# Optimization experiments

Hardware: AMD Instinct MI355X
Metric: run time of the kernel (lower is better)

## Reference

```python
import jax, jax.numpy as jnp
import numpy as np

CH = 96          # channels
E = 2 * CH       # expand_ratio * channels = 192
S = 16           # ssm_state_dim
LN_EPS = 1e-3    # keras LayerNormalization default epsilon


def setup_inputs() -> dict:
    key = jax.random.key(0)
    ks = jax.random.split(key, 8)
    inputs = jax.random.normal(ks[0], (8, 128, 128, CH), dtype=jnp.float32)
    scale = 0.05
    return {
        "inputs": inputs,
        "ln_gamma": jnp.ones((CH,), jnp.float32),
        "ln_beta": jnp.zeros((CH,), jnp.float32),
        "W_expand": jax.random.normal(ks[1], (CH, E), jnp.float32) * scale,
        "W_gate": jax.random.normal(ks[2], (CH, E), jnp.float32) * scale,
        "A": jax.random.normal(ks[3], (E, S), jnp.float32) * scale,
        "B": jax.random.normal(ks[4], (E, S), jnp.float32) * scale,
        "C": jax.random.normal(ks[5], (E, S), jnp.float32) * scale,
        "D": jnp.zeros((E,), jnp.float32),
        "W_out": jax.random.normal(ks[6], (E, CH), jnp.float32) * scale,
    }


def _layernorm(x, gamma, beta):
    mean = jnp.mean(x, axis=-1, keepdims=True)
    var = jnp.mean(jnp.square(x - mean), axis=-1, keepdims=True)
    return (x - mean) / jnp.sqrt(var + LN_EPS) * gamma + beta


def _ssm_scan(u, A, B, C, D):
    # u: [Bn, H, W, E]; diagonal linear recurrence along W with per-(channel,state) params.
    Bn, H, W, Ech = u.shape
    u_t = jnp.moveaxis(u, 2, 0)  # [W, Bn, H, E]

    def step(state, u_w):  # state: [Bn, H, E, S], u_w: [Bn, H, E]
        st = state * A + u_w[..., None] * B               # [Bn, H, E, S]
        # Faithful to the TF code: u*D is broadcast over the state dim
        # before the sum, contributing S * u * D.
        y = jnp.sum(st * C, axis=-1) + S * u_w * D        # [Bn, H, E]
        return st, y

    init = jnp.zeros((Bn, H, Ech, S), dtype=u.dtype)
    _, y = jax.lax.scan(step, init, u_t)                  # y: [W, Bn, H, E]
    return jnp.moveaxis(y, 0, 2)                          # [Bn, H, W, E]


def reference(inputs, ln_gamma, ln_beta, W_expand, W_gate, A, B, C, D, W_out):
    x = _layernorm(inputs, ln_gamma, ln_beta)
    x_proj = jnp.einsum("bhwc,ce->bhwe", x, W_expand)
    gate = jax.nn.sigmoid(jnp.einsum("bhwc,ce->bhwe", x, W_gate))
    ssm_out = _ssm_scan(x_proj, A, B, C, D)
    gated = gate * ssm_out
    return jnp.einsum("bhwe,ec->bhwc", gated, W_out)
```

## Files before the change

kernel.cpp:

```cpp
#include <hip/hip_runtime.h>
#include <math.h>

#define CHN 96
#define EC 192
#define SS 16
#define WPIX 128
#define TILE 16
#define HPX 64
#define NTILES (HPX / TILE)
#define KT 8
#define HALO (KT - 1)
#define NT 192

__global__ void prep_scale(const float* __restrict__ We,
                           const float* __restrict__ Wg,
                           const float* __restrict__ gamma,
                           float* __restrict__ WeP,
                           float* __restrict__ WgP) {
    const int c = blockIdx.x;
    const int e = threadIdx.x;
    const float g = gamma[c];
    WeP[c * EC + e] = g * We[c * EC + e];
    WgP[c * EC + e] = g * Wg[c * EC + e];
}

__global__ void prep_sums(const float* __restrict__ We,
                          const float* __restrict__ Wg,
                          const float* __restrict__ beta,
                          const float* __restrict__ WeP,
                          const float* __restrict__ WgP,
                          float* __restrict__ se, float* __restrict__ be,
                          float* __restrict__ sg, float* __restrict__ bg) {
    const int e = threadIdx.x;
    float s1 = 0.f, b1 = 0.f, s2 = 0.f, b2 = 0.f;
    for (int c = 0; c < CHN; ++c) {
        s1 += WeP[c * EC + e];
        s2 += WgP[c * EC + e];
        b1 += beta[c] * We[c * EC + e];
        b2 += beta[c] * Wg[c * EC + e];
    }
    se[e] = s1; be[e] = b1; sg[e] = s2; bg[e] = b2;
}

#define LOADW(W, c4) {                                         \
    W##0 = wep[((c4) * 4 + 0) * EC]; W##1 = wep[((c4) * 4 + 1) * EC]; \
    W##2 = wep[((c4) * 4 + 2) * EC]; W##3 = wep[((c4) * 4 + 3) * EC]; \
    W##4 = wgp[((c4) * 4 + 0) * EC]; W##5 = wgp[((c4) * 4 + 1) * EC]; \
    W##6 = wgp[((c4) * 4 + 2) * EC]; W##7 = wgp[((c4) * 4 + 3) * EC]; }

#define FMAB(W, c4) {                                          \
    _Pragma("unroll")                                          \
    for (int w = 0; w < TILE; ++w) {                           \
        float4 xv = *(const float4*)(xtile + w * CHN + (c4) * 4); \
        accp[w] = fmaf(xv.x, W##0, accp[w]);                   \
        accp[w] = fmaf(xv.y, W##1, accp[w]);                   \
        accp[w] = fmaf(xv.z, W##2, accp[w]);                   \
        accp[w] = fmaf(xv.w, W##3, accp[w]);                   \
        accg[w] = fmaf(xv.x, W##4, accg[w]);                   \
        accg[w] = fmaf(xv.y, W##5, accg[w]);                   \
        accg[w] = fmaf(xv.z, W##6, accg[w]);                   \
        accg[w] = fmaf(xv.w, W##7, accg[w]); } }

#define LOADO(W, ch) {                                         \
    _Pragma("unroll")                                          \
    for (int k = 0; k < 16; ++k) W[k] = Wo[((ch) * 16 + k) * CHN + co]; }

#define FMAO(W, ch) {                                          \
    _Pragma("unroll")                                          \
    for (int j = 0; j < 8; ++j) {                              \
        const float* gp_ = &gs[wgr * 8 + j][(ch) * 16];        \
        _Pragma("unroll")                                      \
        for (int k4 = 0; k4 < 4; ++k4) {                       \
            float4 gv = *(const float4*)(gp_ + k4 * 4);        \
            acco[j] = fmaf(gv.x, W[k4 * 4 + 0], acco[j]);      \
            acco[j] = fmaf(gv.y, W[k4 * 4 + 1], acco[j]);      \
            acco[j] = fmaf(gv.z, W[k4 * 4 + 2], acco[j]);      \
            acco[j] = fmaf(gv.w, W[k4 * 4 + 3], acco[j]); } } }

__global__ __launch_bounds__(NT, 6)
void mamba_fused(const float* __restrict__ in,
                 const float* __restrict__ WeP,
                 const float* __restrict__ WgP,
                 const float* __restrict__ sev,
                 const float* __restrict__ bev,
                 const float* __restrict__ sgv,
                 const float* __restrict__ bgv,
                 const float* __restrict__ Ap,
                 const float* __restrict__ Bp,
                 const float* __restrict__ Cp,
                 const float* __restrict__ Dp,
                 const float* __restrict__ Wo,
                 float* __restrict__ out) {
    __shared__ float gs[TILE][EC];
    __shared__ float2 stats[TILE];
    __shared__ float2 stats_h[HALO];

    const int t = threadIdx.x;
    const int row  = blockIdx.x >> 1;
    const int half = blockIdx.x & 1;
    const float* inrow = in + (size_t)row * WPIX * CHN;

    const int e = t;
    const float* wep = WeP + e;
    const float* wgp = WgP + e;
    const float se_r = sev[e], be_r = bev[e], sg_r = sgv[e], bg_r = bgv[e];

    float h[KT];
    {
        #pragma unroll
        for (int k = 0; k < KT; ++k) h[k] = 0.f;
        for (int s = 0; s < SS; ++s) {
            const float a = Ap[e * SS + s];
            float p = Bp[e * SS + s] * Cp[e * SS + s];
            #pragma unroll
            for (int k = 0; k < KT; ++k) { h[k] += p; p *= a; }
        }
        h[0] += (float)SS * Dp[e];
    }

    const int px  = t >> 3;
    const int ln  = t & 7;
    const int co  = t % CHN;
    const int wgr = t / CHN;

    float hist[HALO];
    #pragma unroll
    for (int i = 0; i < HALO; ++i) hist[i] = 0.f;

    if (half == 1) {
        if (t < 8 * HALO) {
            const float* pin = inrow + (size_t)(HPX - HALO + px) * CHN + ln * 12;
            float4 v0 = *(const float4*)(pin + 0);
            float4 v1 = *(const float4*)(pin + 4);
            float4 v2 = *(const float4*)(pin + 8);
            float sum = v0.x + v0.y + v0.z + v0.w
                      + v1.x + v1.y + v1.z + v1.w
                      + v2.x + v2.y + v2.z + v2.w;
            float sq = v0.x*v0.x + v0.y*v0.y + v0.z*v0.z + v0.w*v0.w
                     + v1.x*v1.x + v1.y*v1.y + v1.z*v1.z + v1.w*v1.w
                     + v2.x*v2.x + v2.y*v2.y + v2.z*v2.z + v2.w*v2.w;
            #pragma unroll
            for (int m = 1; m < 8; m <<= 1) {
                sum += __shfl_xor(sum, m);
                sq  += __shfl_xor(sq,  m);
            }
            const float mean = sum * (1.f / CHN);
            const float var  = sq * (1.f / CHN) - mean * mean;
            const float rstd = rsqrtf(var + 1e-3f);
            if (ln == 0) stats_h[px] = make_float2(rstd, mean * rstd);
        }
        __syncthreads();

        float accph[HALO];
        #pragma unroll
        for (int j = 0; j < HALO; ++j) accph[j] = 0.f;
        const float* xh = inrow + (size_t)(HPX - HALO) * CHN;
        for (int c4 = 0; c4 < 24; ++c4) {
            const float w0_ = wep[(c4 * 4 + 0) * EC];
            const float w1_ = wep[(c4 * 4 + 1) * EC];
            const float w2_ = wep[(c4 * 4 + 2) * EC];
            const float w3_ = wep[(c4 * 4 + 3) * EC];
            #pragma unroll
            for (int j = 0; j < HALO; ++j) {
                float4 xv = *(const float4*)(xh + j * CHN + c4 * 4);
                accph[j] = fmaf(xv.x, w0_, accph[j]);
                accph[j] = fmaf(xv.y, w1_, accph[j]);
                accph[j] = fmaf(xv.z, w2_, accph[j]);
                accph[j] = fmaf(xv.w, w3_, accph[j]);
            }
        }
        #pragma unroll
        for (int j = 0; j < HALO; ++j) {
            const float2 sp = stats_h[j];
            hist[j] = fmaf(accph[j], sp.x, fmaf(-sp.y, se_r, be_r));
        }
    }

    for (int tile = 0; tile < NTILES; ++tile) {
        const int w0 = half * HPX + tile * TILE;
        const float* xtile = inrow + (size_t)w0 * CHN;

        if (t < 128) {
            const float* pin = xtile + (size_t)px * CHN + ln * 12;
            float4 v0 = *(const float4*)(pin + 0);
            float4 v1 = *(const float4*)(pin + 4);
            float4 v2 = *(const float4*)(pin + 8);
            float sum = v0.x + v0.y + v0.z + v0.w
                      + v1.x + v1.y + v1.z + v1.w
                      + v2.x + v2.y + v2.z + v2.w;
            float sq = v0.x*v0.x + v0.y*v0.y + v0.z*v0.z + v0.w*v0.w
                     + v1.x*v1.x + v1.y*v1.y + v1.z*v1.z + v1.w*v1.w
                     + v2.x*v2.x + v2.y*v2.y + v2.z*v2.z + v2.w*v2.w;
            #pragma unroll
            for (int m = 1; m < 8; m <<= 1) {
                sum += __shfl_xor(sum, m);
                sq  += __shfl_xor(sq,  m);
            }
            const float mean = sum * (1.f / CHN);
            const float var  = sq * (1.f / CHN) - mean * mean;
            const float rstd = rsqrtf(var + 1e-3f);
            if (ln == 0) stats[px] = make_float2(rstd, mean * rstd);
        }
        __syncthreads();

        float accp[TILE], accg[TILE];
        #pragma unroll
        for (int w = 0; w < TILE; ++w) { accp[w] = 0.f; accg[w] = 0.f; }

        {
            float wA0, wA1, wA2, wA3, wA4, wA5, wA6, wA7;
            float wB0, wB1, wB2, wB3, wB4, wB5, wB6, wB7;
            LOADW(wA, 0);
            for (int c4 = 0; c4 < 24; c4 += 2) {
                LOADW(wB, c4 + 1);
                FMAB(wA, c4);
                const int nx = (c4 + 2 < 24) ? c4 + 2 : 0;
                LOADW(wA, nx);
                FMAB(wB, c4 + 1);
            }
        }

        #pragma unroll
        for (int w = 0; w < TILE; ++w) {
            const float2 sp = stats[w];
            accp[w] = fmaf(accp[w], sp.x, fmaf(-sp.y, se_r, be_r));
        }
        #pragma unroll
        for (int w = 0; w < TILE; ++w) {
            const float2 sp = stats[w];
            const float gpre = fmaf(accg[w], sp.x, fmaf(-sp.y, sg_r, bg_r));
            float y = 0.f;
            #pragma unroll
            for (int k = 0; k < KT; ++k) {
                const int idx = w - k;
                const float uv = (idx >= 0) ? accp[idx] : hist[idx + HALO];
                y = fmaf(h[k], uv, y);
            }
            const float g = 1.f / (1.f + __expf(-gpre));
            gs[w][e] = g * y;
        }
        #pragma unroll
        for (int i = 0; i < HALO; ++i) hist[i] = accp[TILE - HALO + i];
        __syncthreads();

        {
            float acco[8];
            #pragma unroll
            for (int j = 0; j < 8; ++j) acco[j] = 0.f;

            float WA[16], WB[16];
            LOADO(WA, 0);
            for (int ch = 0; ch < 12; ch += 2) {
                LOADO(WB, ch + 1);
                FMAO(WA, ch);
                const int nx = (ch + 2 < 12) ? ch + 2 : 0;
                LOADO(WA, nx);
                FMAO(WB, ch + 1);
            }

            #pragma unroll
            for (int j = 0; j < 8; ++j) {
                out[((size_t)row * WPIX + w0 + wgr * 8 + j) * CHN + co] = acco[j];
            }
        }
    }
}

extern "C" void kernel_launch(void* const* d_in, const int* in_sizes, int n_in,
                              void* d_out, int out_size, void* d_ws, size_t ws_size,
                              hipStream_t stream) {
    const float* in    = (const float*)d_in[0];
    const float* gamma = (const float*)d_in[1];
    const float* beta  = (const float*)d_in[2];
    const float* We    = (const float*)d_in[3];
    const float* Wg    = (const float*)d_in[4];
    const float* Ap    = (const float*)d_in[5];
    const float* Bp    = (const float*)d_in[6];
    const float* Cp    = (const float*)d_in[7];
    const float* Dp    = (const float*)d_in[8];
    const float* Wo    = (const float*)d_in[9];
    float* out = (float*)d_out;

    float* wsf = (float*)d_ws;
    float* WeP = wsf;
    float* WgP = wsf + 18432;
    float* se  = wsf + 36864;
    float* be  = wsf + 37056;
    float* sg  = wsf + 37248;
    float* bg  = wsf + 37440;

    prep_scale<<<dim3(CHN), dim3(EC), 0, stream>>>(We, Wg, gamma, WeP, WgP);
    prep_sums<<<dim3(1), dim3(EC), 0, stream>>>(We, Wg, beta, WeP, WgP, se, be, sg, bg);
    mamba_fused<<<dim3(2 * 8 * 128), dim3(NT), 0, stream>>>(
        in, WeP, WgP, se, be, sg, bg, Ap, Bp, Cp, Dp, Wo, out);
}
```

Baseline: 421.1 us.

## Merge both row halves into one 384-thread block and use nontemporal output stores

```diff
diff --git a/kernel.cpp b/kernel.cpp
--- a/kernel.cpp
+++ b/kernel.cpp
@@ -10,7 +10,8 @@
 #define NTILES (HPX / TILE)
 #define KT 8
 #define HALO (KT - 1)
-#define NT 192
+#define GT 192
+#define NT 384
 
 __global__ void prep_scale(const float* __restrict__ We,
                            const float* __restrict__ Wg,
@@ -68,7 +69,7 @@
 #define FMAO(W, ch) {                                          \
     _Pragma("unroll")                                          \
     for (int j = 0; j < 8; ++j) {                              \
-        const float* gp_ = &gs[wgr * 8 + j][(ch) * 16];        \
+        const float* gp_ = &gsl[wgr * 8 + j][(ch) * 16];       \
         _Pragma("unroll")                                      \
         for (int k4 = 0; k4 < 4; ++k4) {                       \
             float4 gv = *(const float4*)(gp_ + k4 * 4);        \
@@ -91,16 +92,20 @@
                  const float* __restrict__ Dp,
                  const float* __restrict__ Wo,
                  float* __restrict__ out) {
-    __shared__ float gs[TILE][EC];
-    __shared__ float2 stats[TILE];
+    __shared__ float gs[2][TILE][EC];
+    __shared__ float2 stats[2][TILE];
     __shared__ float2 stats_h[HALO];
 
-    const int t = threadIdx.x;
-    const int row  = blockIdx.x >> 1;
-    const int half = blockIdx.x & 1;
+    const int t   = threadIdx.x;
+    const int grp = t / GT;
+    const int tl  = t % GT;
+    const int row = blockIdx.x;
     const float* inrow = in + (size_t)row * WPIX * CHN;
 
-    const int e = t;
+    float (*gsl)[EC]  = gs[grp];
+    float2*   statsl  = stats[grp];
+
+    const int e = tl;
     const float* wep = WeP + e;
     const float* wgp = WgP + e;
     const float se_r = sev[e], be_r = bev[e], sg_r = sgv[e], bg_r = bgv[e];
@@ -118,39 +123,39 @@
         h[0] += (float)SS * Dp[e];
     }
 
-    const int px  = t >> 3;
-    const int ln  = t & 7;
-    const int co  = t % CHN;
-    const int wgr = t / CHN;
+    const int px  = tl >> 3;
+    const int ln  = tl & 7;
+    const int co  = tl % CHN;
+    const int wgr = tl / CHN;
 
     float hist[HALO];
     #pragma unroll
     for (int i = 0; i < HALO; ++i) hist[i] = 0.f;
 
-    if (half == 1) {
-        if (t < 8 * HALO) {
-            const float* pin = inrow + (size_t)(HPX - HALO + px) * CHN + ln * 12;
-            float4 v0 = *(const float4*)(pin + 0);
-            float4 v1 = *(const float4*)(pin + 4);
-            float4 v2 = *(const float4*)(pin + 8);
-            float sum = v0.x + v0.y + v0.z + v0.w
-                      + v1.x + v1.y + v1.z + v1.w
-                      + v2.x + v2.y + v2.z + v2.w;
-            float sq = v0.x*v0.x + v0.y*v0.y + v0.z*v0.z + v0.w*v0.w
-                     + v1.x*v1.x + v1.y*v1.y + v1.z*v1.z + v1.w*v1.w
-                     + v2.x*v2.x + v2.y*v2.y + v2.z*v2.z + v2.w*v2.w;
-            #pragma unroll
-            for (int m = 1; m < 8; m <<= 1) {
-                sum += __shfl_xor(sum, m);
-                sq  += __shfl_xor(sq,  m);
-            }
-            const float mean = sum * (1.f / CHN);
-            const float var  = sq * (1.f / CHN) - mean * mean;
-            const float rstd = rsqrtf(var + 1e-3f);
-            if (ln == 0) stats_h[px] = make_float2(rstd, mean * rstd);
-        }
-        __syncthreads();
-
+    if (grp == 1 && tl < 8 * HALO) {
+        const float* pin = inrow + (size_t)(HPX - HALO + px) * CHN + ln * 12;
+        float4 v0 = *(const float4*)(pin + 0);
+        float4 v1 = *(const float4*)(pin + 4);
+        float4 v2 = *(const float4*)(pin + 8);
+        float sum = v0.x + v0.y + v0.z + v0.w
+                  + v1.x + v1.y + v1.z + v1.w
+                  + v2.x + v2.y + v2.z + v2.w;
+        float sq = v0.x*v0.x + v0.y*v0.y + v0.z*v0.z + v0.w*v0.w
+                 + v1.x*v1.x + v1.y*v1.y + v1.z*v1.z + v1.w*v1.w
+                 + v2.x*v2.x + v2.y*v2.y + v2.z*v2.z + v2.w*v2.w;
+        #pragma unroll
+        for (int m = 1; m < 8; m <<= 1) {
+            sum += __shfl_xor(sum, m);
+            sq  += __shfl_xor(sq,  m);
+        }
+        const float mean = sum * (1.f / CHN);
+        const float var  = sq * (1.f / CHN) - mean * mean;
+        const float rstd = rsqrtf(var + 1e-3f);
+        if (ln == 0) stats_h[px] = make_float2(rstd, mean * rstd);
+    }
+    __syncthreads();
+
+    if (grp == 1) {
         float accph[HALO];
         #pragma unroll
         for (int j = 0; j < HALO; ++j) accph[j] = 0.f;
@@ -177,10 +182,10 @@
     }
 
     for (int tile = 0; tile < NTILES; ++tile) {
-        const int w0 = half * HPX + tile * TILE;
+        const int w0 = grp * HPX + tile * TILE;
         const float* xtile = inrow + (size_t)w0 * CHN;
 
-        if (t < 128) {
+        if (tl < 128) {
             const float* pin = xtile + (size_t)px * CHN + ln * 12;
             float4 v0 = *(const float4*)(pin + 0);
             float4 v1 = *(const float4*)(pin + 4);
@@ -199,7 +204,7 @@
             const float mean = sum * (1.f / CHN);
             const float var  = sq * (1.f / CHN) - mean * mean;
             const float rstd = rsqrtf(var + 1e-3f);
-            if (ln == 0) stats[px] = make_float2(rstd, mean * rstd);
+            if (ln == 0) statsl[px] = make_float2(rstd, mean * rstd);
         }
         __syncthreads();
 
@@ -222,12 +227,12 @@
 
         #pragma unroll
         for (int w = 0; w < TILE; ++w) {
-            const float2 sp = stats[w];
+            const float2 sp = statsl[w];
             accp[w] = fmaf(accp[w], sp.x, fmaf(-sp.y, se_r, be_r));
         }
         #pragma unroll
         for (int w = 0; w < TILE; ++w) {
-            const float2 sp = stats[w];
+            const float2 sp = statsl[w];
             const float gpre = fmaf(accg[w], sp.x, fmaf(-sp.y, sg_r, bg_r));
             float y = 0.f;
             #pragma unroll
@@ -237,7 +242,7 @@
                 y = fmaf(h[k], uv, y);
             }
             const float g = 1.f / (1.f + __expf(-gpre));
-            gs[w][e] = g * y;
+            gsl[w][e] = g * y;
         }
         #pragma unroll
         for (int i = 0; i < HALO; ++i) hist[i] = accp[TILE - HALO + i];
@@ -260,7 +265,9 @@
 
             #pragma unroll
             for (int j = 0; j < 8; ++j) {
-                out[((size_t)row * WPIX + w0 + wgr * 8 + j) * CHN + co] = acco[j];
+                __builtin_nontemporal_store(
+                    acco[j],
+                    &out[((size_t)row * WPIX + w0 + wgr * 8 + j) * CHN + co]);
             }
         }
     }
@@ -291,6 +298,6 @@
 
     prep_scale<<<dim3(CHN), dim3(EC), 0, stream>>>(We, Wg, gamma, WeP, WgP);
     prep_sums<<<dim3(1), dim3(EC), 0, stream>>>(We, Wg, beta, WeP, WgP, se, be, sg, bg);
-    mamba_fused<<<dim3(2 * 8 * 128), dim3(NT), 0, stream>>>(
+    mamba_fused<<<dim3(8 * 128), dim3(NT), 0, stream>>>(
         in, WeP, WgP, se, be, sg, bg, Ap, Bp, Cp, Dp, Wo, out);
 }
```

After: 1.145 ms. 2.72x slower.
